# Kernel tuning notes

Measured on AMD Instinct MI355X. Metric: run time of the kernel, lower is better.

The kernel has to match this reference:

```python
import jax, jax.numpy as jnp
import numpy as np

MAX_REL = 16  # max_relative_position (keys == values)


def _relative_positions(T, max_pos):
    r = jnp.arange(T)
    dist = r[None, :] - r[:, None]          # [T, T], k - q
    return jnp.clip(dist, -max_pos, max_pos) + max_pos


def setup_inputs() -> dict:
    key = jax.random.key(0)
    ks = jax.random.split(key, 5)
    B, H, T, D = 4, 16, 1024, 64
    V = 2 * MAX_REL + 1
    return {
        "q": jax.random.normal(ks[0], (B, H, T, D), jnp.float32),
        "k": jax.random.normal(ks[1], (B, H, T, D), jnp.float32),
        "v": jax.random.normal(ks[2], (B, H, T, D), jnp.float32),
        "emb_k": jax.random.normal(ks[3], (V, D), jnp.float32),
        "emb_v": jax.random.normal(ks[4], (V, D), jnp.float32),
    }


def reference(q, k, v, emb_k, emb_v):
    # q,k,v: [B,H,T,D]; emb_*: [2*MAX_REL+1, D]
    T = q.shape[2]
    D = k.shape[-1]
    rel_idx = _relative_positions(T, MAX_REL)          # [T,T]
    rel_k = emb_k[rel_idx]                             # [T,T,D]
    rel_v = emb_v[rel_idx]                             # [T,T,D]

    # content-content + content-position logits
    logits = jnp.einsum('bhtd,bhsd->bhts', q, k)
    logits = logits + jnp.einsum('bhtd,tsd->bhts', q, rel_k)
    logits = logits * (1.0 / jnp.sqrt(jnp.float32(D)))

    attn = jax.nn.softmax(logits, axis=-1)             # [B,H,T,T]
    out = jnp.einsum('bhts,bhsd->bhtd', attn, v)
    out = out + jnp.einsum('bhts,tsd->bhtd', attn, rel_v)
    return out, attn
```

## Files before the change

kernel.cpp:

```cpp
#include <hip/hip_runtime.h>
#include <hip/hip_bf16.h>

#define TT 1024
#define DD 64
#define MAXREL 16
#define NV 33
#define QBLK 16
#define SCALE 0.125f
#define BH 64

typedef short bf16x8 __attribute__((ext_vector_type(8)));
typedef short bf16x4 __attribute__((ext_vector_type(4)));
typedef float f32x4 __attribute__((ext_vector_type(4)));

#define SBAR() __builtin_amdgcn_sched_barrier(0)
#define WAITV(N)   __builtin_amdgcn_s_waitcnt(0x0F70 | (N))
#define WAITLGKM() __builtin_amdgcn_s_waitcnt(0xC07F)

static __device__ inline void gload16(const void* g, void* l) {
    __builtin_amdgcn_global_load_lds(
        (const __attribute__((address_space(1))) void*)g,
        (__attribute__((address_space(3))) void*)l, 16, 0, 0);
}

static __device__ inline short f2bf(float f) {
    __hip_bfloat16 h = __float2bfloat16(f);
    return *(short*)&h;
}
static __device__ inline float bf2f(short s) {
    union { unsigned u; float f; } x;
    x.u = ((unsigned)(unsigned short)s) << 16;
    return x.f;
}
static __device__ inline bf16x8 pack8(float4 a, float4 b) {
    bf16x8 r;
    r[0]=f2bf(a.x); r[1]=f2bf(a.y); r[2]=f2bf(a.z); r[3]=f2bf(a.w);
    r[4]=f2bf(b.x); r[5]=f2bf(b.y); r[6]=f2bf(b.z); r[7]=f2bf(b.w);
    return r;
}

__global__ __launch_bounds__(256)
void convk_kernel(const float* __restrict__ src, short* __restrict__ dst) {
    size_t i = (size_t)blockIdx.x * 256 + threadIdx.x;
    const float4* s = (const float4*)(src + i * 8);
    *(bf16x8*)(dst + i * 8) = pack8(s[0], s[1]);
}

__global__ __launch_bounds__(256)
void transv_kernel(const float* __restrict__ v, short* __restrict__ vt) {
    int bh = blockIdx.x >> 4;
    int st = blockIdx.x & 15;
    int wave = threadIdx.x >> 6, lane = threadIdx.x & 63;
    int s0 = st * 64 + wave * 16;
    const float* vp = v + ((size_t)bh * TT + s0) * DD + lane;
    bf16x8 lo, hi;
    #pragma unroll
    for (int e = 0; e < 8; ++e) lo[e] = f2bf(vp[(size_t)e * DD]);
    #pragma unroll
    for (int e = 0; e < 8; ++e) hi[e] = f2bf(vp[(size_t)(e + 8) * DD]);
    short* dp = vt + ((size_t)bh * DD + lane) * TT + s0;
    *(bf16x8*)dp = lo;
    *(bf16x8*)(dp + 8) = hi;
}

__global__ __launch_bounds__(512)
void relattn_kernel(const float* __restrict__ q_g,
                    const short* __restrict__ kb,
                    const short* __restrict__ vt,
                    const float* __restrict__ ek_g,
                    const float* __restrict__ ev_g,
                    float* __restrict__ out_g,
                    float* __restrict__ attn_g) {
    __shared__ __align__(16) char pbuf[QBLK * 2048];
    __shared__ __align__(16) char kstage[8 * 4096];
    __shared__ float pair_lds[4][16][16];
    __shared__ float qe_lds[QBLK * NV];
    __shared__ float w_lds[QBLK * NV];
    __shared__ float psum_lds[QBLK][8];
    __shared__ float psuf_lds[QBLK][8];
    __shared__ float pmid_lds[QBLK][8];
    __shared__ float inv_lds[QBLK];

    const int t    = threadIdx.x;
    const int bid  = blockIdx.x;
    const int wg   = ((bid & 7) << 9) | (bid >> 3);
    const int bh   = wg >> 6;
    const int q0   = (wg & 63) * QBLK;
    const int w    = t >> 6;
    const int lane = t & 63;
    const int lr   = lane & 15;
    const int akg  = lane >> 4;
    const int srl  = lane >> 3;
    const int sqg  = (lane & 7) ^ srl;

    const short* kgbase = kb + (size_t)bh * TT * DD;
    char* kst = kstage + w * 4096;

    auto KSTAGE = [&](int B, int NT) {
        const int s0 = w * 128 + NT * 16;
        gload16(kgbase + (size_t)(s0 + srl) * 64 + sqg * 8,     kst + B * 2048);
        gload16(kgbase + (size_t)(s0 + 8 + srl) * 64 + sqg * 8, kst + B * 2048 + 1024);
    };

    bf16x8 qF0, qF1;
    {
        const float* qp = q_g + ((size_t)bh * TT + q0 + lr) * DD + akg * 8;
        float4 a = *(const float4*)qp,        b = *(const float4*)(qp + 4);
        float4 c = *(const float4*)(qp + 32), d = *(const float4*)(qp + 36);
        qF0 = pack8(a, b); qF1 = pack8(c, d);
    }

    KSTAGE(0, 0); KSTAGE(1, 1);

    for (int i = t; i < QBLK * NV; i += 512) w_lds[i] = 0.f;
    if (w < 3) {
        int v = w * 16 + lr; if (v > 32) v = 32;
        const float* ep = ek_g + v * DD + akg * 8;
        float4 a = *(const float4*)ep,        b = *(const float4*)(ep + 4);
        float4 c = *(const float4*)(ep + 32), d = *(const float4*)(ep + 36);
        bf16x8 eF0 = pack8(a, b), eF1 = pack8(c, d);
        f32x4 qacc = {0.f, 0.f, 0.f, 0.f};
        qacc = __builtin_amdgcn_mfma_f32_16x16x32_bf16(eF0, qF0, qacc, 0, 0, 0);
        qacc = __builtin_amdgcn_mfma_f32_16x16x32_bf16(eF1, qF1, qacc, 0, 0, 0);
        #pragma unroll
        for (int j = 0; j < 4; ++j) {
            int vv = w * 16 + akg * 4 + j;
            if (vv < NV) qe_lds[lr * NV + vv] = __expf(qacc[j] * SCALE);
        }
    }
    __syncthreads();

    {
        const int tq = q0 + lr;
        const int X  = (lr & 7) << 4;
        const float eqe_lo = qe_lds[lr * NV];
        const float eqe_hi = qe_lds[lr * NV + 32];
        float sum = 0.f, suff = 0.f, msum = 0.f;

        auto CVALU = [&](f32x4 acc, int nt) {
            const int sb = w * 128 + nt * 16 + akg * 4;
            float ex0 = __expf(acc[0] * SCALE), ex1 = __expf(acc[1] * SCALE);
            float ex2 = __expf(acc[2] * SCALE), ex3 = __expf(acc[3] * SCALE);
            float e0, e1, e2, e3;
            if (sb >= tq + MAXREL) {
                e0 = ex0 * eqe_hi; e1 = ex1 * eqe_hi;
                e2 = ex2 * eqe_hi; e3 = ex3 * eqe_hi;
                float csum = (e0 + e1) + (e2 + e3);
                sum += csum; suff += csum;
            } else if (sb + 3 <= tq - MAXREL) {
                e0 = ex0 * eqe_lo; e1 = ex1 * eqe_lo;
                e2 = ex2 * eqe_lo; e3 = ex3 * eqe_lo;
                sum += (e0 + e1) + (e2 + e3);
            } else {
                float ee[4]; float exs[4] = {ex0, ex1, ex2, ex3};
                #pragma unroll
                for (int j = 0; j < 4; ++j) {
                    int dr = sb + j - tq;
                    int dc = dr < -MAXREL ? -MAXREL : (dr > MAXREL ? MAXREL : dr);
                    float v = exs[j] * qe_lds[lr * NV + dc + MAXREL];
                    ee[j] = v;
                    sum += v;
                    if (dr >= MAXREL) suff += v;
                    if (dr > -MAXREL && dr < MAXREL) {
                        w_lds[lr * NV + dr + MAXREL] = v;
                        msum += v;
                    }
                }
                e0 = ee[0]; e1 = ee[1]; e2 = ee[2]; e3 = ee[3];
            }
            bf16x4 p4;
            p4[0] = f2bf(e0); p4[1] = f2bf(e1);
            p4[2] = f2bf(e2); p4[3] = f2bf(e3);
            *(bf16x4*)(pbuf + lr * 2048 + ((2 * sb) ^ X)) = p4;
        };

        auto MFMA2 = [&](bf16x8 kf0, bf16x8 kf1) {
            f32x4 acc = {0.f, 0.f, 0.f, 0.f};
            acc = __builtin_amdgcn_mfma_f32_16x16x32_bf16(kf0, qF0, acc, 0, 0, 0);
            acc = __builtin_amdgcn_mfma_f32_16x16x32_bf16(kf1, qF1, acc, 0, 0, 0);
            return acc;
        };

        f32x4 aA, aB;
        #define CITER(B, NT, W, PF, AC, AP, NP) \
            WAITV(W); SBAR(); \
            { bf16x8 kf0 = *(const bf16x8*)(kst + (B)*2048 + lr*128 + ((((akg))  ^(lr&7)) << 4)); \
              bf16x8 kf1 = *(const bf16x8*)(kst + (B)*2048 + lr*128 + ((((akg)+4)^(lr&7)) << 4)); \
              if ((NP) >= 0) CVALU(AP, NP); \
              WAITLGKM(); SBAR(); \
              if (PF) KSTAGE((B), (NT) + 2); \
              AC = MFMA2(kf0, kf1); } \
            SBAR()
        CITER(0, 0, 2, 1, aA, aB, -1);
        CITER(1, 1, 2, 1, aB, aA,  0);
        CITER(0, 2, 2, 1, aA, aB,  1);
        CITER(1, 3, 2, 1, aB, aA,  2);
        CITER(0, 4, 2, 1, aA, aB,  3);
        CITER(1, 5, 2, 1, aB, aA,  4);
        CITER(0, 6, 2, 0, aA, aB,  5);
        CITER(1, 7, 0, 0, aB, aA,  6);
        CVALU(aB, 7);
        #undef CITER

        {
            WAITLGKM(); SBAR();
            const short* vgbase = vt + ((size_t)bh * DD + (w & 3) * 16) * TT;
            const int S0 = (w >> 2) * 8;
            gload16(vgbase + (size_t)srl * TT + S0 * 64 + sqg * 8,           kst);
            gload16(vgbase + (size_t)(8 + srl) * TT + S0 * 64 + sqg * 8,     kst + 1024);
            gload16(vgbase + (size_t)srl * TT + (S0 + 1) * 64 + sqg * 8,     kst + 2048);
            gload16(vgbase + (size_t)(8 + srl) * TT + (S0 + 1) * 64 + sqg * 8, kst + 3072);
        }

        sum  += __shfl_xor(sum, 16);  sum  += __shfl_xor(sum, 32);
        suff += __shfl_xor(suff, 16); suff += __shfl_xor(suff, 32);
        msum += __shfl_xor(msum, 16); msum += __shfl_xor(msum, 32);
        if (lane < 16) {
            psum_lds[lr][w] = sum;
            psuf_lds[lr][w] = suff;
            pmid_lds[lr][w] = msum;
        }
    }
    __syncthreads();

    if (t < QBLK) {
        float s = 0.f, sf = 0.f, sm = 0.f;
        #pragma unroll
        for (int i = 0; i < 8; ++i) {
            s  += psum_lds[t][i];
            sf += psuf_lds[t][i];
            sm += pmid_lds[t][i];
        }
        inv_lds[t] = 1.0f / s;
        w_lds[t * NV]      = s - sf - sm;
        w_lds[t * NV + 32] = sf;
    }
    __syncthreads();

    {
        const int dt = w & 3;
        const int sh = w >> 2;
        const int S0 = sh * 8;
        const int lc = lane & 15;
        const int dcol = dt * 16 + lc;
        const char* pb = pbuf + lc * 2048;
        const int X = (lc & 7) << 4;
        char* vst = kst;
        const short* vgbase = vt + ((size_t)bh * DD + dt * 16) * TT;
        f32x4 acc0 = {0.f, 0.f, 0.f, 0.f};
        f32x4 acc1 = {0.f, 0.f, 0.f, 0.f};

        auto VSTAGE = [&](int B, int S) {
            gload16(vgbase + (size_t)srl * TT + S * 64 + sqg * 8,       vst + B * 2048);
            gload16(vgbase + (size_t)(8 + srl) * TT + S * 64 + sqg * 8, vst + B * 2048 + 1024);
        };

        #define FITER(B, S, W, PF, AC) \
            WAITV(W); SBAR(); \
            { bf16x8 vf0 = *(const bf16x8*)(vst + (B)*2048 + lc*128 + ((((akg))  ^(lc&7)) << 4)); \
              bf16x8 vf1 = *(const bf16x8*)(vst + (B)*2048 + lc*128 + ((((akg)+4)^(lc&7)) << 4)); \
              bf16x8 a0 = *(const bf16x8*)(pb + (((2*(S))*64     + akg*16) ^ X)); \
              bf16x8 a1 = *(const bf16x8*)(pb + (((2*(S)+1)*64   + akg*16) ^ X)); \
              WAITLGKM(); SBAR(); \
              if (PF) VSTAGE((B), (S) + 2); \
              AC = __builtin_amdgcn_mfma_f32_16x16x32_bf16(a0, vf0, AC, 0, 0, 0); \
              AC = __builtin_amdgcn_mfma_f32_16x16x32_bf16(a1, vf1, AC, 0, 0, 0); } \
            SBAR()
        FITER(0, S0 + 0, 2, 1, acc0);  FITER(1, S0 + 1, 2, 1, acc1);
        FITER(0, S0 + 2, 2, 1, acc0);  FITER(1, S0 + 3, 2, 1, acc1);
        FITER(0, S0 + 4, 2, 1, acc0);  FITER(1, S0 + 5, 2, 1, acc1);
        FITER(0, S0 + 6, 2, 0, acc0);  FITER(1, S0 + 7, 0, 0, acc1);
        #undef FITER

        f32x4 acc;
        acc[0] = acc0[0] + acc1[0]; acc[1] = acc0[1] + acc1[1];
        acc[2] = acc0[2] + acc1[2]; acc[3] = acc0[3] + acc1[3];

        if (sh == 1) {
            #pragma unroll
            for (int j = 0; j < 4; ++j)
                pair_lds[dt][akg * 4 + j][lc] = acc[j];
        }
        __syncthreads();

        if (sh == 0) {
            const int rb = akg * 4;
            float o0 = acc[0] + pair_lds[dt][rb + 0][lc];
            float o1 = acc[1] + pair_lds[dt][rb + 1][lc];
            float o2 = acc[2] + pair_lds[dt][rb + 2][lc];
            float o3 = acc[3] + pair_lds[dt][rb + 3][lc];
            #pragma unroll 8
            for (int v = 0; v < NV; ++v) {
                float ev = ev_g[v * DD + dcol];
                o0 += w_lds[(rb + 0) * NV + v] * ev;
                o1 += w_lds[(rb + 1) * NV + v] * ev;
                o2 += w_lds[(rb + 2) * NV + v] * ev;
                o3 += w_lds[(rb + 3) * NV + v] * ev;
            }
            float* op = out_g + ((size_t)bh * TT + q0 + rb) * DD + dcol;
            op[0 * DD] = o0 * inv_lds[rb + 0];
            op[1 * DD] = o1 * inv_lds[rb + 1];
            op[2 * DD] = o2 * inv_lds[rb + 2];
            op[3 * DD] = o3 * inv_lds[rb + 3];
        }
    }

    {
        float* ab = attn_g + ((size_t)bh * TT + q0) * TT;
        #pragma unroll
        for (int j = 0; j < 2; ++j) {
            const int r = w * 2 + j;
            const float inv = inv_lds[r];
            const int X = (r & 7) << 4;
            #pragma unroll
            for (int i = 0; i < 4; ++i) {
                bf16x4 p4 = *(const bf16x4*)(pbuf + r * 2048 + ((8 * lane + 512 * i) ^ X));
                f32x4 o;
                o[0] = bf2f(p4[0]) * inv; o[1] = bf2f(p4[1]) * inv;
                o[2] = bf2f(p4[2]) * inv; o[3] = bf2f(p4[3]) * inv;
                __builtin_nontemporal_store(o, (f32x4*)(ab + (size_t)r * TT + lane * 4 + 256 * i));
            }
        }
    }
}

extern "C" void kernel_launch(void* const* d_in, const int* in_sizes, int n_in,
                              void* d_out, int out_size, void* d_ws, size_t ws_size,
                              hipStream_t stream) {
    const float* q  = (const float*)d_in[0];
    const float* k  = (const float*)d_in[1];
    const float* v  = (const float*)d_in[2];
    const float* ek = (const float*)d_in[3];
    const float* ev = (const float*)d_in[4];
    float* out  = (float*)d_out;
    float* attn = out + (size_t)BH * TT * DD;

    short* kbuf = (short*)d_ws;
    short* vtb  = kbuf + (size_t)BH * TT * DD;

    convk_kernel<<<dim3(2048), dim3(256), 0, stream>>>(k, kbuf);
    transv_kernel<<<dim3(1024), dim3(256), 0, stream>>>(v, vtb);
    relattn_kernel<<<dim3(4096), dim3(512), 0, stream>>>(q, kbuf, vtb, ek, ev, out, attn);
}
```

Before: 118.9 us.

## Fuse K/V prep kernels and interleave attn stores with PV MFMA loop

Merges the K bf16 conversion and the V transpose into one prep kernel that transposes V through an LDS tile with coalesced reads and writes, removing one launch and the strided V reads. In the main kernel, the normalized attention-probability stores are moved out of the epilogue and spread one per iteration across the P·V MFMA loop, so the large attn write traffic overlaps with compute. This adds LDS reads and global stores inside the tightly scheduled loop, which may disturb the wait-count and scheduling assumptions.

After: 120.1 us. About the same (+1.0%).

```diff
diff --git a/kernel.cpp b/kernel.cpp
--- a/kernel.cpp
+++ b/kernel.cpp
@@ -40,27 +40,47 @@
 }
 
 __global__ __launch_bounds__(256)
-void convk_kernel(const float* __restrict__ src, short* __restrict__ dst) {
-    size_t i = (size_t)blockIdx.x * 256 + threadIdx.x;
-    const float4* s = (const float4*)(src + i * 8);
-    *(bf16x8*)(dst + i * 8) = pack8(s[0], s[1]);
-}
-
-__global__ __launch_bounds__(256)
-void transv_kernel(const float* __restrict__ v, short* __restrict__ vt) {
-    int bh = blockIdx.x >> 4;
-    int st = blockIdx.x & 15;
-    int wave = threadIdx.x >> 6, lane = threadIdx.x & 63;
-    int s0 = st * 64 + wave * 16;
-    const float* vp = v + ((size_t)bh * TT + s0) * DD + lane;
-    bf16x8 lo, hi;
-    #pragma unroll
-    for (int e = 0; e < 8; ++e) lo[e] = f2bf(vp[(size_t)e * DD]);
-    #pragma unroll
-    for (int e = 0; e < 8; ++e) hi[e] = f2bf(vp[(size_t)(e + 8) * DD]);
-    short* dp = vt + ((size_t)bh * DD + lane) * TT + s0;
-    *(bf16x8*)dp = lo;
-    *(bf16x8*)(dp + 8) = hi;
+void prep_kernel(const float* __restrict__ k, const float* __restrict__ v,
+                 short* __restrict__ kbuf, short* __restrict__ vt) {
+    __shared__ short tile[64][66];
+    const int bh = blockIdx.x >> 4;
+    const int s0 = (blockIdx.x & 15) * 64;
+    const int t  = threadIdx.x;
+    const int r  = t >> 2;
+    const int g  = t & 3;
+
+    {
+        const float* kp = k + ((size_t)bh * TT + s0 + r) * DD + g * 16;
+        float4 a0 = *(const float4*)(kp);
+        float4 a1 = *(const float4*)(kp + 4);
+        float4 a2 = *(const float4*)(kp + 8);
+        float4 a3 = *(const float4*)(kp + 12);
+        short* dp = kbuf + ((size_t)bh * TT + s0 + r) * DD + g * 16;
+        *(bf16x8*)dp       = pack8(a0, a1);
+        *(bf16x8*)(dp + 8) = pack8(a2, a3);
+    }
+    {
+        const float* vp = v + ((size_t)bh * TT + s0 + r) * DD + g * 16;
+        float4 a0 = *(const float4*)(vp);
+        float4 a1 = *(const float4*)(vp + 4);
+        float4 a2 = *(const float4*)(vp + 8);
+        float4 a3 = *(const float4*)(vp + 12);
+        bf16x8 b0 = pack8(a0, a1), b1 = pack8(a2, a3);
+        #pragma unroll
+        for (int j = 0; j < 8; ++j) {
+            tile[g * 16 + j][r]     = b0[j];
+            tile[g * 16 + 8 + j][r] = b1[j];
+        }
+    }
+    __syncthreads();
+    {
+        const int d = t >> 2, c = t & 3;
+        bf16x8 o0 = *(const bf16x8*)&tile[d][c * 16];
+        bf16x8 o1 = *(const bf16x8*)&tile[d][c * 16 + 8];
+        short* dp = vt + ((size_t)bh * DD + d) * TT + s0 + c * 16;
+        *(bf16x8*)dp       = o0;
+        *(bf16x8*)(dp + 8) = o1;
+    }
 }
 
 __global__ __launch_bounds__(512)
@@ -247,6 +267,7 @@
         const int X = (lc & 7) << 4;
         char* vst = kst;
         const short* vgbase = vt + ((size_t)bh * DD + dt * 16) * TT;
+        float* ab = attn_g + ((size_t)bh * TT + q0) * TT;
         f32x4 acc0 = {0.f, 0.f, 0.f, 0.f};
         f32x4 acc1 = {0.f, 0.f, 0.f, 0.f};
 
@@ -255,9 +276,22 @@
             gload16(vgbase + (size_t)(8 + srl) * TT + S * 64 + sqg * 8, vst + B * 2048 + 1024);
         };
 
-        #define FITER(B, S, W, PF, AC) \
+        auto ASTORE = [&](int ST) {
+            const int r_ = w * 2 + (ST >> 2);
+            const int i_ = ST & 3;
+            const float inv_ = inv_lds[r_];
+            const int Xr = (r_ & 7) << 4;
+            bf16x4 p4 = *(const bf16x4*)(pbuf + r_ * 2048 + ((8 * lane + 512 * i_) ^ Xr));
+            f32x4 o;
+            o[0] = bf2f(p4[0]) * inv_; o[1] = bf2f(p4[1]) * inv_;
+            o[2] = bf2f(p4[2]) * inv_; o[3] = bf2f(p4[3]) * inv_;
+            __builtin_nontemporal_store(o, (f32x4*)(ab + (size_t)r_ * TT + lane * 4 + 256 * i_));
+        };
+
+        #define FITER(B, S, W, PF, AC, ST) \
             WAITV(W); SBAR(); \
-            { bf16x8 vf0 = *(const bf16x8*)(vst + (B)*2048 + lc*128 + ((((akg))  ^(lc&7)) << 4)); \
+            { ASTORE(ST); \
+              bf16x8 vf0 = *(const bf16x8*)(vst + (B)*2048 + lc*128 + ((((akg))  ^(lc&7)) << 4)); \
               bf16x8 vf1 = *(const bf16x8*)(vst + (B)*2048 + lc*128 + ((((akg)+4)^(lc&7)) << 4)); \
               bf16x8 a0 = *(const bf16x8*)(pb + (((2*(S))*64     + akg*16) ^ X)); \
               bf16x8 a1 = *(const bf16x8*)(pb + (((2*(S)+1)*64   + akg*16) ^ X)); \
@@ -266,10 +300,10 @@
               AC = __builtin_amdgcn_mfma_f32_16x16x32_bf16(a0, vf0, AC, 0, 0, 0); \
               AC = __builtin_amdgcn_mfma_f32_16x16x32_bf16(a1, vf1, AC, 0, 0, 0); } \
             SBAR()
-        FITER(0, S0 + 0, 2, 1, acc0);  FITER(1, S0 + 1, 2, 1, acc1);
-        FITER(0, S0 + 2, 2, 1, acc0);  FITER(1, S0 + 3, 2, 1, acc1);
-        FITER(0, S0 + 4, 2, 1, acc0);  FITER(1, S0 + 5, 2, 1, acc1);
-        FITER(0, S0 + 6, 2, 0, acc0);  FITER(1, S0 + 7, 0, 0, acc1);
+        FITER(0, S0 + 0, 2, 1, acc0, 0);  FITER(1, S0 + 1, 2, 1, acc1, 1);
+        FITER(0, S0 + 2, 2, 1, acc0, 2);  FITER(1, S0 + 3, 2, 1, acc1, 3);
+        FITER(0, S0 + 4, 2, 1, acc0, 4);  FITER(1, S0 + 5, 2, 1, acc1, 5);
+        FITER(0, S0 + 6, 2, 0, acc0, 6);  FITER(1, S0 + 7, 0, 0, acc1, 7);
         #undef FITER
 
         f32x4 acc;
@@ -304,24 +338,6 @@
             op[3 * DD] = o3 * inv_lds[rb + 3];
         }
     }
-
-    {
-        float* ab = attn_g + ((size_t)bh * TT + q0) * TT;
-        #pragma unroll
-        for (int j = 0; j < 2; ++j) {
-            const int r = w * 2 + j;
-            const float inv = inv_lds[r];
-            const int X = (r & 7) << 4;
-            #pragma unroll
-            for (int i = 0; i < 4; ++i) {
-                bf16x4 p4 = *(const bf16x4*)(pbuf + r * 2048 + ((8 * lane + 512 * i) ^ X));
-                f32x4 o;
-                o[0] = bf2f(p4[0]) * inv; o[1] = bf2f(p4[1]) * inv;
-                o[2] = bf2f(p4[2]) * inv; o[3] = bf2f(p4[3]) * inv;
-                __builtin_nontemporal_store(o, (f32x4*)(ab + (size_t)r * TT + lane * 4 + 256 * i));
-            }
-        }
-    }
 }
 
 extern "C" void kernel_launch(void* const* d_in, const int* in_sizes, int n_in,
@@ -338,7 +354,6 @@
     short* kbuf = (short*)d_ws;
     short* vtb  = kbuf + (size_t)BH * TT * DD;
 
-    convk_kernel<<<dim3(2048), dim3(256), 0, stream>>>(k, kbuf);
-    transv_kernel<<<dim3(1024), dim3(256), 0, stream>>>(v, vtb);
+    prep_kernel<<<dim3(1024), dim3(256), 0, stream>>>(k, v, kbuf, vtb);
     relattn_kernel<<<dim3(4096), dim3(512), 0, stream>>>(q, kbuf, vtb, ek, ev, out, attn);
 }
```
